# Performance work log

Hardware: AMD Instinct MI355X
Metric: run time of the kernel (lower is better)

## Reference

```python
import jax, jax.numpy as jnp
import numpy as np

B, L, D = 8, 1024, 768
H, W, Dd = 16, 16, 4          # token grid, H*W*Dd == L
N, R, K = 16, 48, 4           # d_state, dt_rank, d_conv
EPS = 1e-5


def _physical_pos_embed(batch_params, has_velocity):
    # physical coords [B, L, 3]: (distance, angle, velocity/time)
    h_idx = jnp.arange(H, dtype=jnp.float32)[None, :, None, None]
    w_idx = jnp.arange(W, dtype=jnp.float32)[None, None, :, None]
    d_idx = jnp.arange(Dd, dtype=jnp.float32)[None, None, None, :]
    rres = batch_params[:, 0][:, None, None, None]
    ares = batch_params[:, 1][:, None, None, None]
    vres = batch_params[:, 2][:, None, None, None]
    zero = jnp.zeros((1, H, W, Dd), jnp.float32)
    dist = h_idx * rres + zero
    ang = (w_idx - W / 2) * ares + zero
    vel = jnp.where(has_velocity[:, None, None, None],
                    (d_idx - Dd / 2) * vres, d_idx * vres) + zero
    coords = jnp.stack([dist, ang, vel], axis=-1).reshape(B, L, 3)
    mx = coords.max(axis=1, keepdims=True)
    mn = coords.min(axis=1, keepdims=True)
    rng = mx - mn
    rng = jnp.where(rng > 0, rng, jnp.ones_like(rng))
    coords = (coords - mn) / rng
    # sincos embed: D/3 = 256 dims per coord (even -> pure sin/cos)
    fdim = D // 3
    omega = jnp.arange(fdim // 2, dtype=jnp.float32) / (fdim / 2.0)
    omega = 1.0 / (10000.0 ** omega)                      # [128]
    out = jnp.einsum('blc,f->blcf', coords, omega)        # [B,L,3,128]
    emb = jnp.concatenate([jnp.sin(out), jnp.cos(out)], axis=-1)  # [B,L,3,256]
    return emb.reshape(B, L, D)


def _rmsnorm(x, w):
    return x * jax.lax.rsqrt(jnp.mean(x * x, axis=-1, keepdims=True) + EPS) * w


def _mamba(h, in_proj_w, in_proj_b, conv_w, conv_b, x_proj_w,
           dt_proj_w, dt_proj_b, A_log, D_param, out_proj_w, out_proj_b):
    xz = h @ in_proj_w.T + in_proj_b                      # [B,L,2D]
    x_in, z = xz[..., :D], xz[..., D:]
    # causal depthwise conv1d, kernel K
    xp = jnp.pad(x_in, ((0, 0), (K - 1, 0), (0, 0)))
    x_conv = sum(xp[:, k:k + L, :] * conv_w[:, 0, k] for k in range(K))
    x_conv = jax.nn.silu(x_conv + conv_b)
    x_dbl = x_conv @ x_proj_w.T                           # [B,L,R+2N]
    dt, Bm, Cm = x_dbl[..., :R], x_dbl[..., R:R + N], x_dbl[..., R + N:]
    dt = jax.nn.softplus(dt @ dt_proj_w.T + dt_proj_b)    # [B,L,D]
    A = -jnp.exp(A_log)                                   # [D,N]
    dA = jnp.exp(dt[..., None] * A)                       # [B,L,D,N]
    dBx = dt[..., None] * Bm[:, :, None, :] * x_conv[..., None]

    def step(hst, inp):
        dA_t, dBx_t, C_t = inp
        hst = dA_t * hst + dBx_t                          # [B,D,N]
        y_t = jnp.einsum('bdn,bn->bd', hst, C_t)
        return hst, y_t

    h0 = jnp.zeros((B, D, N), x_in.dtype)
    _, ys = jax.lax.scan(step, h0, (dA.transpose(1, 0, 2, 3),
                                    dBx.transpose(1, 0, 2, 3),
                                    Cm.transpose(1, 0, 2)))
    y = ys.transpose(1, 0, 2) + D_param * x_conv          # [B,L,D]
    y = y * jax.nn.silu(z)
    return y @ out_proj_w.T + out_proj_b


def reference(x, batch_params, has_velocity, norm_w, in_proj_w, in_proj_b,
              conv_w, conv_b, x_proj_w, dt_proj_w, dt_proj_b, A_log,
              D_param, out_proj_w, out_proj_b):
    pos = _physical_pos_embed(batch_params, has_velocity)
    residual = x + pos                                    # ARBlock residual
    hidden = _rmsnorm(residual, norm_w)
    hidden = _mamba(hidden, in_proj_w, in_proj_b, conv_w, conv_b, x_proj_w,
                    dt_proj_w, dt_proj_b, A_log, D_param,
                    out_proj_w, out_proj_b)
    return hidden + residual


def setup_inputs():
    key = jax.random.key(0)
    ks = jax.random.split(key, 12)
    s = 0.02
    return {
        'x': jax.random.normal(ks[0], (B, L, D), jnp.float32),
        'batch_params': jax.random.uniform(ks[1], (B, 4), jnp.float32, 0.01, 1.0),
        'has_velocity': jax.random.randint(ks[2], (B,), 0, 2) > 0,
        'norm_w': jnp.ones((D,), jnp.float32),
        'in_proj_w': jax.random.normal(ks[3], (2 * D, D), jnp.float32) * s,
        'in_proj_b': jnp.zeros((2 * D,), jnp.float32),
        'conv_w': jax.random.normal(ks[4], (D, 1, K), jnp.float32) * 0.3,
        'conv_b': jnp.zeros((D,), jnp.float32),
        'x_proj_w': jax.random.normal(ks[5], (R + 2 * N, D), jnp.float32) * s,
        'dt_proj_w': jax.random.normal(ks[6], (D, R), jnp.float32) * s,
        'dt_proj_b': jax.random.normal(ks[7], (D,), jnp.float32) * 0.1,
        'A_log': jnp.log(jax.random.uniform(ks[8], (D, N), jnp.float32, 1.0, 16.0)),
        'D_param': jnp.ones((D,), jnp.float32),
        'out_proj_w': jax.random.normal(ks[9], (D, D), jnp.float32) * s,
        'out_proj_b': jnp.zeros((D,), jnp.float32),
    }
```

## Files before the change

kernel.cpp:

```cpp
#include <hip/hip_runtime.h>
#include <math.h>

#define BB 8
#define LL 1024
#define DD 768
#define NNs 16
#define RR 48

typedef __attribute__((ext_vector_type(8))) short bf16x8;
typedef __attribute__((ext_vector_type(4))) float f32x4;

__device__ __forceinline__ float silu_f(float v) { return v / (1.0f + __expf(-v)); }

__device__ __forceinline__ short f2bf(float f) {
    union { float f; unsigned u; } v; v.f = f;
    unsigned r = (v.u + 0x7fffu + ((v.u >> 16) & 1u)) >> 16;
    return (short)r;
}

__device__ __forceinline__ void async16(const void* g, void* l) {
    __builtin_amdgcn_global_load_lds((const __attribute__((address_space(1))) void*)g,
                                     (__attribute__((address_space(3))) void*)l,
                                     16, 0, 0);
}

__global__ __launch_bounds__(256) void k_cvt(const float* __restrict__ src,
                                             short* __restrict__ dst, int n4) {
    int i = blockIdx.x * 256 + threadIdx.x;
    if (i < n4) {
        float4 v = ((const float4*)src)[i];
        short4 o = { f2bf(v.x), f2bf(v.y), f2bf(v.z), f2bf(v.w) };
        ((short4*)dst)[i] = o;
    }
}

__global__ __launch_bounds__(256) void k_pos_rms(const float* __restrict__ x,
                                                 const float* __restrict__ norm_w,
                                                 float* __restrict__ res,
                                                 short* __restrict__ hidb) {
    int row = blockIdx.x;
    int l = row & (LL - 1);
    int d3 = l & 3;
    int w = (l >> 2) & 15;
    int h = l >> 6;
    float coord[3] = { h * (1.0f / 15.0f), w * (1.0f / 15.0f), d3 * (1.0f / 3.0f) };
    const float LOG1E4 = 9.210340371976184f;
    int t = threadIdx.x;
    float r[3];
    float s = 0.0f;
#pragma unroll
    for (int i = 0; i < 3; i++) {
        int j = t + i * 256;
        int c = j >> 8;
        int fp = j & 255;
        int f = fp & 127;
        float omega = __expf(-(f * (1.0f / 128.0f)) * LOG1E4);
        float arg = coord[c] * omega;
        float pv = (fp < 128) ? __sinf(arg) : __cosf(arg);
        float rv = x[(size_t)row * DD + j] + pv;
        r[i] = rv;
        s += rv * rv;
    }
#pragma unroll
    for (int off = 32; off; off >>= 1) s += __shfl_xor(s, off, 64);
    __shared__ float ls[4];
    if ((t & 63) == 0) ls[t >> 6] = s;
    __syncthreads();
    s = ls[0] + ls[1] + ls[2] + ls[3];
    float rs = rsqrtf(s * (1.0f / DD) + 1e-5f);
#pragma unroll
    for (int i = 0; i < 3; i++) {
        int j = t + i * 256;
        res[(size_t)row * DD + j] = r[i];
        hidb[(size_t)row * DD + j] = f2bf(r[i] * rs * norm_w[j]);
    }
}

template <int EPI, bool AF32>
__global__ __launch_bounds__(256) void gemm_mfma(const void* __restrict__ Ap,
                                                 const short* __restrict__ Bw,
                                                 int Kd,
                                                 const float* __restrict__ bias,
                                                 const float* __restrict__ resid,
                                                 float* __restrict__ C0,
                                                 float* __restrict__ C1) {
    __shared__ short As[4096];
    __shared__ short Bs[4096];
    int m0 = blockIdx.y * 128;
    int n0 = blockIdx.x * 128;
    int tid = threadIdx.x;
    int lane = tid & 63, wave = tid >> 6;
    int q = lane >> 4, r = lane & 15;
    int wm = wave >> 1, wn = wave & 1;

    const size_t Kb = (size_t)Kd * 2;
    const char* gB0 = (const char*)Bw + (size_t)(n0 + wave * 16 + r) * Kb + q * 16;
    const char* gB1 = gB0 + 64 * Kb;
    char* lB0 = (char*)Bs + wave * 1024;
    char* lB1 = lB0 + 4096;
    const char* gA0 = nullptr; const char* gA1 = nullptr;
    char* lA0 = nullptr; char* lA1 = nullptr;
    if (!AF32) {
        gA0 = (const char*)Ap + (size_t)(m0 + wave * 16 + r) * Kb + q * 16;
        gA1 = gA0 + 64 * Kb;
        lA0 = (char*)As + wave * 1024;
        lA1 = lA0 + 4096;
    }

    f32x4 acc[4][4] = {};

    for (int k0 = 0; k0 < Kd; k0 += 32) {
        if (AF32) {
            const float* Af = (const float*)Ap;
#pragma unroll
            for (int p = 0; p < 2; p++) {
                int m = m0 + (p * 4 + wave) * 16 + r;
                const float* src = Af + (size_t)m * Kd + k0 + q * 8;
                float4 v0 = *(const float4*)src;
                float4 v1 = *(const float4*)(src + 4);
                bf16x8 pk;
                pk[0] = f2bf(v0.x); pk[1] = f2bf(v0.y);
                pk[2] = f2bf(v0.z); pk[3] = f2bf(v0.w);
                pk[4] = f2bf(v1.x); pk[5] = f2bf(v1.y);
                pk[6] = f2bf(v1.z); pk[7] = f2bf(v1.w);
                *(bf16x8*)&As[p * 2048 + wave * 512 + lane * 8] = pk;
            }
        } else {
            async16(gA0, lA0); async16(gA1, lA1);
            gA0 += 64; gA1 += 64;
        }
        async16(gB0, lB0); async16(gB1, lB1);
        gB0 += 64; gB1 += 64;
        __syncthreads();
        bf16x8 af[4], bf[4];
#pragma unroll
        for (int a = 0; a < 4; a++)
            af[a] = *(const bf16x8*)&As[((wm * 4 + a) * 64 + q * 16 + r) * 8];
#pragma unroll
        for (int b = 0; b < 4; b++)
            bf[b] = *(const bf16x8*)&Bs[((wn * 4 + b) * 64 + q * 16 + r) * 8];
#pragma unroll
        for (int a = 0; a < 4; a++)
#pragma unroll
            for (int b = 0; b < 4; b++)
                acc[a][b] = __builtin_amdgcn_mfma_f32_16x16x32_bf16(
                    af[a], bf[b], acc[a][b], 0, 0, 0);
        __syncthreads();
    }

#pragma unroll
    for (int a = 0; a < 4; a++) {
        int mrow = m0 + (wm * 4 + a) * 16 + q * 4;
#pragma unroll
        for (int b = 0; b < 4; b++) {
            int ncol = n0 + (wn * 4 + b) * 16 + r;
            float bb = bias[ncol];
            if (EPI == 1) {
                float* dst = (ncol < DD) ? (C0 + (size_t)mrow * DD + ncol)
                                         : (C1 + (size_t)mrow * DD + (ncol - DD));
#pragma unroll
                for (int e = 0; e < 4; e++)
                    dst[(size_t)e * DD] = acc[a][b][e] + bb;
            } else {
#pragma unroll
                for (int e = 0; e < 4; e++) {
                    size_t idx = (size_t)(mrow + e) * DD + ncol;
                    C0[idx] = acc[a][b][e] + bb + resid[idx];
                }
            }
        }
    }
}

template <int MODE>
__global__ __launch_bounds__(256) void gemm_nt(const float* __restrict__ A, int lda,
                                               const float* __restrict__ Bw, int ldb,
                                               int N, int Kd,
                                               const float* __restrict__ bias,
                                               float* __restrict__ C0, int ldc) {
    __shared__ __align__(16) float As[16][68];
    __shared__ __align__(16) float Bs[16][68];
    int m0 = blockIdx.y * 64;
    int n0 = blockIdx.x * 64;
    int t = threadIdx.x;
    int tx = t & 15, ty = t >> 4;
    int ar = t >> 2;
    int ak = (t & 3) * 4;
    float acc[4][4] = {};
    for (int k0 = 0; k0 < Kd; k0 += 16) {
        float4 av = *(const float4*)(A + (size_t)(m0 + ar) * lda + k0 + ak);
        int brow = n0 + ar;
        if (brow >= N) brow = N - 1;
        float4 bv = *(const float4*)(Bw + (size_t)brow * ldb + k0 + ak);
        As[ak + 0][ar] = av.x; As[ak + 1][ar] = av.y;
        As[ak + 2][ar] = av.z; As[ak + 3][ar] = av.w;
        Bs[ak + 0][ar] = bv.x; Bs[ak + 1][ar] = bv.y;
        Bs[ak + 2][ar] = bv.z; Bs[ak + 3][ar] = bv.w;
        __syncthreads();
#pragma unroll
        for (int kk = 0; kk < 16; kk++) {
            float4 a4 = *(const float4*)&As[kk][ty * 4];
            float4 b4 = *(const float4*)&Bs[kk][tx * 4];
            float aa[4] = { a4.x, a4.y, a4.z, a4.w };
            float bb[4] = { b4.x, b4.y, b4.z, b4.w };
#pragma unroll
            for (int i = 0; i < 4; i++)
#pragma unroll
                for (int j = 0; j < 4; j++) acc[i][j] += aa[i] * bb[j];
        }
        __syncthreads();
    }
    if (MODE == 0) {
#pragma unroll
        for (int i = 0; i < 4; i++) {
            int m = m0 + ty * 4 + i;
#pragma unroll
            for (int j = 0; j < 4; j++) {
                int n = n0 + tx * 4 + j;
                if (n < N) C0[(size_t)m * ldc + n] = acc[i][j];
            }
        }
    } else {
        float4 bi = *(const float4*)(bias + n0 + tx * 4);
        float bl[4] = { bi.x, bi.y, bi.z, bi.w };
#pragma unroll
        for (int i = 0; i < 4; i++) {
            int m = m0 + ty * 4 + i;
            float v[4];
#pragma unroll
            for (int j = 0; j < 4; j++) {
                float u = acc[i][j] + bl[j];
                v[j] = (u > 20.0f) ? u : log1pf(__expf(u));
            }
            float4 o = { v[0], v[1], v[2], v[3] };
            *(float4*)(C0 + (size_t)m * DD + n0 + tx * 4) = o;
        }
    }
}

__global__ __launch_bounds__(256) void k_conv(const float* __restrict__ xin,
                                              const float* __restrict__ cw,
                                              const float* __restrict__ cb,
                                              float* __restrict__ xc) {
    size_t gid = (size_t)blockIdx.x * 256 + threadIdx.x;
    int d = (int)(gid % DD);
    int bt = (int)(gid / DD);
    int tt = bt & (LL - 1);
    float4 w = ((const float4*)cw)[d];
    const float* p = xin + (size_t)bt * DD + d;
    float acc = cb[d];
    if (tt >= 3) acc += p[-3 * DD] * w.x;
    if (tt >= 2) acc += p[-2 * DD] * w.y;
    if (tt >= 1) acc += p[-1 * DD] * w.z;
    acc += p[0] * w.w;
    xc[gid] = silu_f(acc);
}

__global__ __launch_bounds__(256) void k_scan(const float* __restrict__ dtf,
                                              const float* __restrict__ xc,
                                              const float* __restrict__ xdbl,
                                              const float* __restrict__ A_log,
                                              const float* __restrict__ Dp,
                                              float* __restrict__ zy) {
    __shared__ float Pl[16 * 16 * 16];
    __shared__ float Sl[16 * 16 * 16];
    int b = blockIdx.y;
    int d0 = blockIdx.x * 16;
    int tid = threadIdx.x;
    int dl = tid & 15;
    int c = tid >> 4;
    int d = d0 + dl;

    float Ac[16];
    {
        const float4* al = (const float4*)(A_log + d * NNs);
#pragma unroll
        for (int i = 0; i < 4; i++) {
            float4 v = al[i];
            Ac[i * 4 + 0] = -__expf(v.x); Ac[i * 4 + 1] = -__expf(v.y);
            Ac[i * 4 + 2] = -__expf(v.z); Ac[i * 4 + 3] = -__expf(v.w);
        }
    }
    size_t rb = ((size_t)(b * LL + c * 64)) * DD + d;
    const float* dtp = dtf + rb;
    const float* xcp = xc + rb;
    float* zp = zy + rb;
    const float* xrow = xdbl + ((size_t)(b * LL + c * 64)) * 80 + RR;

    float P[16], S[16];
#pragma unroll
    for (int n = 0; n < 16; n++) { P[n] = 1.0f; S[n] = 0.0f; }
    for (int i = 0; i < 64; i++) {
        float dtv = dtp[(size_t)i * DD];
        float xcv = xcp[(size_t)i * DD];
        float dx = dtv * xcv;
        const float* Br = xrow + i * 80;
#pragma unroll
        for (int qq = 0; qq < 4; qq++) {
            float4 B4 = *(const float4*)(Br + qq * 4);
            float bl[4] = { B4.x, B4.y, B4.z, B4.w };
#pragma unroll
            for (int j = 0; j < 4; j++) {
                int n = qq * 4 + j;
                float e = __expf(dtv * Ac[n]);
                P[n] *= e;
                S[n] = e * S[n] + dx * bl[j];
            }
        }
    }
    {
        float* pw = &Pl[(c * 16 + dl) * 16];
        float* sw = &Sl[(c * 16 + dl) * 16];
#pragma unroll
        for (int qq = 0; qq < 4; qq++) {
            float4 pv = { P[qq * 4], P[qq * 4 + 1], P[qq * 4 + 2], P[qq * 4 + 3] };
            float4 sv = { S[qq * 4], S[qq * 4 + 1], S[qq * 4 + 2], S[qq * 4 + 3] };
            *(float4*)(pw + qq * 4) = pv;
            *(float4*)(sw + qq * 4) = sv;
        }
    }
    __syncthreads();
    {
        int d2 = tid >> 4, n2 = tid & 15;
        float hh = 0.0f;
#pragma unroll
        for (int cc = 0; cc < 16; cc++) {
            int idx = (cc * 16 + d2) * 16 + n2;
            float Pv = Pl[idx], Sv = Sl[idx];
            Pl[idx] = hh;
            hh = Pv * hh + Sv;
        }
    }
    __syncthreads();
    float h[16];
    {
        const float* hr = &Pl[(c * 16 + dl) * 16];
#pragma unroll
        for (int qq = 0; qq < 4; qq++) {
            float4 v = *(const float4*)(hr + qq * 4);
            h[qq * 4] = v.x; h[qq * 4 + 1] = v.y;
            h[qq * 4 + 2] = v.z; h[qq * 4 + 3] = v.w;
        }
    }
    float Dv = Dp[d];
    for (int i = 0; i < 64; i++) {
        float dtv = dtp[(size_t)i * DD];
        float xcv = xcp[(size_t)i * DD];
        float zv  = zp[(size_t)i * DD];
        float dx = dtv * xcv;
        float y = Dv * xcv;
        const float* Br = xrow + i * 80;
#pragma unroll
        for (int qq = 0; qq < 4; qq++) {
            float4 B4 = *(const float4*)(Br + qq * 4);
            float4 C4 = *(const float4*)(Br + 16 + qq * 4);
            float bl[4] = { B4.x, B4.y, B4.z, B4.w };
            float cl[4] = { C4.x, C4.y, C4.z, C4.w };
#pragma unroll
            for (int j = 0; j < 4; j++) {
                int n = qq * 4 + j;
                float e = __expf(dtv * Ac[n]);
                h[n] = e * h[n] + dx * bl[j];
                y += h[n] * cl[j];
            }
        }
        zp[(size_t)i * DD] = y * silu_f(zv);
    }
}

extern "C" void kernel_launch(void* const* d_in, const int* in_sizes, int n_in,
                              void* d_out, int out_size, void* d_ws, size_t ws_size,
                              hipStream_t stream) {
    const float* x      = (const float*)d_in[0];
    const float* norm_w = (const float*)d_in[3];
    const float* in_w   = (const float*)d_in[4];
    const float* in_b   = (const float*)d_in[5];
    const float* conv_w = (const float*)d_in[6];
    const float* conv_b = (const float*)d_in[7];
    const float* xp_w   = (const float*)d_in[8];
    const float* dt_w   = (const float*)d_in[9];
    const float* dt_b   = (const float*)d_in[10];
    const float* A_log  = (const float*)d_in[11];
    const float* Dp     = (const float*)d_in[12];
    const float* out_w  = (const float*)d_in[13];
    const float* out_b  = (const float*)d_in[14];
    float* out = (float*)d_out;

    const size_t S = (size_t)BB * LL * DD;
    float* res   = (float*)d_ws;
    float* slotA = res + S;
    float* slotB = slotA + S;
    float* zf    = slotB + S;
    float* xdbl  = zf + S;
    short* inw_b  = (short*)(xdbl + (size_t)BB * LL * 80);
    short* outw_b = inw_b + 1536 * DD;

    short* hidb = (short*)slotA;
    float* xc   = slotA;
    float* xin  = slotB;
    float* dtf  = slotB;

    const int M = BB * LL;

    k_cvt<<<(1536 * DD / 4 + 255) / 256, 256, 0, stream>>>(in_w, inw_b, 1536 * DD / 4);
    k_cvt<<<(DD * DD / 4 + 255) / 256, 256, 0, stream>>>(out_w, outw_b, DD * DD / 4);

    k_pos_rms<<<M, 256, 0, stream>>>(x, norm_w, res, hidb);

    gemm_mfma<1, false><<<dim3(1536 / 128, M / 128), 256, 0, stream>>>(
        hidb, inw_b, DD, in_b, nullptr, xin, zf);

    k_conv<<<(int)(S / 256), 256, 0, stream>>>(xin, conv_w, conv_b, xc);

    gemm_nt<0><<<dim3(2, M / 64), 256, 0, stream>>>(
        xc, DD, xp_w, DD, RR + 2 * NNs, DD, nullptr, xdbl, 80);

    gemm_nt<2><<<dim3(DD / 64, M / 64), 256, 0, stream>>>(
        xdbl, 80, dt_w, RR, DD, RR, dt_b, dtf, DD);

    k_scan<<<dim3(DD / 16, BB), 256, 0, stream>>>(dtf, xc, xdbl, A_log, Dp, zf);

    gemm_mfma<3, true><<<dim3(DD / 128, M / 128), 256, 0, stream>>>(
        zf, outw_b, DD, out_b, res, out, nullptr);
}
```

Measured before the change: 391.1 us.

## Stage scan inputs through LDS with async global-to-LDS loads

The selective-scan kernel now loads dt, conv output, z and the B/C rows for eight timesteps per chunk into shared memory with 16-byte global_load_lds transfers, then computes from LDS. Before, each thread issued its own strided scalar loads with a stride of the model width. The change also folds log2(e) into A so the kernel calls exp2f instead of __expf. The aim is coalesced, wider loads for a latency-bound scan. The cost is a larger shared buffer and two barriers per chunk, which may reduce occupancy.

Result: slower. 450.0 us (+15.1%).

```diff
diff --git a/kernel.cpp b/kernel.cpp
--- a/kernel.cpp
+++ b/kernel.cpp
@@ -262,61 +262,75 @@
                                               const float* __restrict__ A_log,
                                               const float* __restrict__ Dp,
                                               float* __restrict__ zy) {
-    __shared__ float Pl[16 * 16 * 16];
-    __shared__ float Sl[16 * 16 * 16];
+    __shared__ float buf[10240];
     int b = blockIdx.y;
     int d0 = blockIdx.x * 16;
     int tid = threadIdx.x;
+    int lane = tid & 63, wave = tid >> 6;
     int dl = tid & 15;
     int c = tid >> 4;
     int d = d0 + dl;
 
-    float Ac[16];
+    float Ac2[16];
     {
         const float4* al = (const float4*)(A_log + d * NNs);
 #pragma unroll
         for (int i = 0; i < 4; i++) {
             float4 v = al[i];
-            Ac[i * 4 + 0] = -__expf(v.x); Ac[i * 4 + 1] = -__expf(v.y);
-            Ac[i * 4 + 2] = -__expf(v.z); Ac[i * 4 + 3] = -__expf(v.w);
-        }
-    }
-    size_t rb = ((size_t)(b * LL + c * 64)) * DD + d;
-    const float* dtp = dtf + rb;
-    const float* xcp = xc + rb;
-    float* zp = zy + rb;
-    const float* xrow = xdbl + ((size_t)(b * LL + c * 64)) * 80 + RR;
+            Ac2[i * 4 + 0] = -__expf(v.x) * 1.44269504f;
+            Ac2[i * 4 + 1] = -__expf(v.y) * 1.44269504f;
+            Ac2[i * 4 + 2] = -__expf(v.z) * 1.44269504f;
+            Ac2[i * 4 + 3] = -__expf(v.w) * 1.44269504f;
+        }
+    }
+    const float* xb = xdbl + (size_t)b * LL * 80;
+    size_t rowbase = (size_t)b * LL;
+
+    int r0 = wave * 16 + (lane >> 2);
+    int lc = (lane & 3) * 16;
 
     float P[16], S[16];
 #pragma unroll
     for (int n = 0; n < 16; n++) { P[n] = 1.0f; S[n] = 0.0f; }
-    for (int i = 0; i < 64; i++) {
-        float dtv = dtp[(size_t)i * DD];
-        float xcv = xcp[(size_t)i * DD];
-        float dx = dtv * xcv;
-        const float* Br = xrow + i * 80;
-#pragma unroll
-        for (int qq = 0; qq < 4; qq++) {
-            float4 B4 = *(const float4*)(Br + qq * 4);
-            float bl[4] = { B4.x, B4.y, B4.z, B4.w };
-#pragma unroll
-            for (int j = 0; j < 4; j++) {
-                int n = qq * 4 + j;
-                float e = __expf(dtv * Ac[n]);
-                P[n] *= e;
-                S[n] = e * S[n] + dx * bl[j];
-            }
-        }
+    for (int g = 0; g < 64; g += 8) {
+#pragma unroll
+        for (int p = 0; p < 2; p++) {
+            int rr = r0 + p * 64;
+            int t = (rr >> 3) * 64 + g + (rr & 7);
+            char* dbase = (char*)buf + p * 4096 + wave * 1024;
+            async16((const char*)(dtf + (rowbase + t) * DD + d0) + lc, dbase);
+            async16((const char*)(xc + (rowbase + t) * DD + d0) + lc, dbase + 8192);
+            async16((const char*)(xb + (size_t)t * 80 + RR) + lc, dbase + 16384);
+        }
+        __syncthreads();
+        for (int i = 0; i < 8; i++) {
+            int ro = (c * 8 + i) * 16;
+            float dtv = buf[ro + dl];
+            float xcv = buf[2048 + ro + dl];
+            float dx = dtv * xcv;
+#pragma unroll
+            for (int qq = 0; qq < 4; qq++) {
+                float4 B4 = *(const float4*)&buf[4096 + ro + qq * 4];
+                float bl[4] = { B4.x, B4.y, B4.z, B4.w };
+#pragma unroll
+                for (int j = 0; j < 4; j++) {
+                    int n = qq * 4 + j;
+                    float e = exp2f(dtv * Ac2[n]);
+                    P[n] *= e;
+                    S[n] = e * S[n] + dx * bl[j];
+                }
+            }
+        }
+        __syncthreads();
     }
     {
-        float* pw = &Pl[(c * 16 + dl) * 16];
-        float* sw = &Sl[(c * 16 + dl) * 16];
+        int base = (c * 16 + dl) * 16;
 #pragma unroll
         for (int qq = 0; qq < 4; qq++) {
             float4 pv = { P[qq * 4], P[qq * 4 + 1], P[qq * 4 + 2], P[qq * 4 + 3] };
             float4 sv = { S[qq * 4], S[qq * 4 + 1], S[qq * 4 + 2], S[qq * 4 + 3] };
-            *(float4*)(pw + qq * 4) = pv;
-            *(float4*)(sw + qq * 4) = sv;
+            *(float4*)&buf[base + qq * 4] = pv;
+            *(float4*)&buf[4096 + base + qq * 4] = sv;
         }
     }
     __syncthreads();
@@ -326,15 +340,15 @@
 #pragma unroll
         for (int cc = 0; cc < 16; cc++) {
             int idx = (cc * 16 + d2) * 16 + n2;
-            float Pv = Pl[idx], Sv = Sl[idx];
-            Pl[idx] = hh;
+            float Pv = buf[idx], Sv = buf[4096 + idx];
+            buf[idx] = hh;
             hh = Pv * hh + Sv;
         }
     }
     __syncthreads();
     float h[16];
     {
-        const float* hr = &Pl[(c * 16 + dl) * 16];
+        const float* hr = &buf[(c * 16 + dl) * 16];
 #pragma unroll
         for (int qq = 0; qq < 4; qq++) {
             float4 v = *(const float4*)(hr + qq * 4);
@@ -342,29 +356,46 @@
             h[qq * 4 + 2] = v.z; h[qq * 4 + 3] = v.w;
         }
     }
+    __syncthreads();
     float Dv = Dp[d];
-    for (int i = 0; i < 64; i++) {
-        float dtv = dtp[(size_t)i * DD];
-        float xcv = xcp[(size_t)i * DD];
-        float zv  = zp[(size_t)i * DD];
-        float dx = dtv * xcv;
-        float y = Dv * xcv;
-        const float* Br = xrow + i * 80;
-#pragma unroll
-        for (int qq = 0; qq < 4; qq++) {
-            float4 B4 = *(const float4*)(Br + qq * 4);
-            float4 C4 = *(const float4*)(Br + 16 + qq * 4);
-            float bl[4] = { B4.x, B4.y, B4.z, B4.w };
-            float cl[4] = { C4.x, C4.y, C4.z, C4.w };
-#pragma unroll
-            for (int j = 0; j < 4; j++) {
-                int n = qq * 4 + j;
-                float e = __expf(dtv * Ac[n]);
-                h[n] = e * h[n] + dx * bl[j];
-                y += h[n] * cl[j];
-            }
-        }
-        zp[(size_t)i * DD] = y * silu_f(zv);
+    for (int g = 0; g < 64; g += 8) {
+#pragma unroll
+        for (int p = 0; p < 2; p++) {
+            int rr = r0 + p * 64;
+            int t = (rr >> 3) * 64 + g + (rr & 7);
+            char* dbase = (char*)buf + p * 4096 + wave * 1024;
+            async16((const char*)(dtf + (rowbase + t) * DD + d0) + lc, dbase);
+            async16((const char*)(xc + (rowbase + t) * DD + d0) + lc, dbase + 8192);
+            async16((const char*)(zy + (rowbase + t) * DD + d0) + lc, dbase + 16384);
+            async16((const char*)(xb + (size_t)t * 80 + RR) + lc, dbase + 24576);
+            async16((const char*)(xb + (size_t)t * 80 + RR + 16) + lc, dbase + 32768);
+        }
+        __syncthreads();
+        for (int i = 0; i < 8; i++) {
+            int ro = (c * 8 + i) * 16;
+            float dtv = buf[ro + dl];
+            float xcv = buf[2048 + ro + dl];
+            float zv  = buf[4096 + ro + dl];
+            float dx = dtv * xcv;
+            float y = Dv * xcv;
+#pragma unroll
+            for (int qq = 0; qq < 4; qq++) {
+                float4 B4 = *(const float4*)&buf[6144 + ro + qq * 4];
+                float4 C4 = *(const float4*)&buf[8192 + ro + qq * 4];
+                float bl[4] = { B4.x, B4.y, B4.z, B4.w };
+                float cl[4] = { C4.x, C4.y, C4.z, C4.w };
+#pragma unroll
+                for (int j = 0; j < 4; j++) {
+                    int n = qq * 4 + j;
+                    float e = exp2f(dtv * Ac2[n]);
+                    h[n] = e * h[n] + dx * bl[j];
+                    y += h[n] * cl[j];
+                }
+            }
+            int t = c * 64 + g + i;
+            zy[(rowbase + t) * DD + d] = y * silu_f(zv);
+        }
+        __syncthreads();
     }
 }
 
```
